# Optimization experiments

Measured on AMD Instinct MI355X. Metric: run time of the kernel, lower is better.

The kernel has to match this reference:

```python
import jax, jax.numpy as jnp
import numpy as np

B_, S_, P_, D_ = 2, 512, 64, 1024
L_ = 4            # n_layer
DI_ = 2 * D_      # d_inner (expand=2)
DS_ = 16          # d_state
DC_ = 4           # d_conv
DR_ = D_ // 16    # dt_rank
PCD_ = 768        # prepend_cond_dim


def setup_inputs() -> dict:
    key = jax.random.key(0)
    ks = jax.random.split(key, 12)
    n = lambda k, s, sc=0.02: jax.random.normal(k, s, dtype=jnp.float32) * sc
    A_log = jnp.log(jnp.broadcast_to(jnp.arange(1, DS_ + 1, dtype=jnp.float32), (L_, DI_, DS_)))
    return {
        'x': jax.random.normal(ks[0], (B_, S_, D_), dtype=jnp.float32),
        'prepend_cond': jax.random.normal(ks[1], (B_, P_, PCD_), dtype=jnp.float32),
        'pre_w1': n(ks[2], (PCD_, D_)),
        'pre_w2': n(ks[3], (D_, D_)),
        'norm_w': jnp.ones((L_, D_), jnp.float32),
        'in_proj_w': n(ks[4], (L_, 2 * DI_, D_)),
        'conv_w': n(ks[5], (L_, DI_, DC_), 0.1),
        'conv_b': jnp.zeros((L_, DI_), jnp.float32),
        'x_proj_w': n(ks[6], (L_, DR_ + 2 * DS_, DI_)),
        'dt_proj_w': n(ks[7], (L_, DI_, DR_), 0.1),
        'dt_proj_b': jax.random.uniform(ks[8], (L_, DI_), jnp.float32, -4.0, -2.0),
        'A_log': A_log,
        'D_param': jnp.ones((L_, DI_), jnp.float32),
        'out_proj_w': n(ks[9], (L_, D_, DI_)),
        'final_norm_w': jnp.ones((D_,), jnp.float32),
    }


def rmsnorm(x, w, eps=1e-5):
    return x * jax.lax.rsqrt(jnp.mean(x * x, axis=-1, keepdims=True) + eps) * w


def mamba_block(x, ip_w, cw, cb, xp_w, dtp_w, dtp_b, A_log, Dp, op_w):
    B, S, _ = x.shape
    xz = jnp.einsum('bsd,ed->bse', x, ip_w)            # [B,S,2*DI]
    xi, z = jnp.split(xz, 2, axis=-1)
    # depthwise causal conv1d along time
    xt = xi.transpose(0, 2, 1)                          # [B,DI,S]
    conv = jax.lax.conv_general_dilated(
        xt, cw[:, None, :], (1,), [(DC_ - 1, 0)], feature_group_count=DI_) + cb[:, None]
    xi = jax.nn.silu(conv.transpose(0, 2, 1))           # [B,S,DI]
    xdbl = jnp.einsum('bse,fe->bsf', xi, xp_w)          # [B,S,DR+2*DS]
    dt, Bm, Cm = jnp.split(xdbl, [DR_, DR_ + DS_], axis=-1)
    dt = jax.nn.softplus(jnp.einsum('bsr,er->bse', dt, dtp_w) + dtp_b)  # [B,S,DI]
    A = -jnp.exp(A_log)                                 # [DI,DS]
    dA = jnp.exp(dt[..., None] * A)                     # [B,S,DI,DS]
    dBu = dt[..., None] * Bm[:, :, None, :] * xi[..., None]

    def step(h, t):
        da, dbu, c = t
        h = da * h + dbu                                # [B,DI,DS]
        return h, jnp.einsum('bes,bs->be', h, c)

    h0 = jnp.zeros((B, DI_, DS_), x.dtype)
    _, ys = jax.lax.scan(step, h0, (dA.transpose(1, 0, 2, 3), dBu.transpose(1, 0, 2, 3), Cm.transpose(1, 0, 2)))
    y = ys.transpose(1, 0, 2) + xi * Dp
    y = y * jax.nn.silu(z)
    return jnp.einsum('bse,de->bsd', y, op_w)


def reference(x, prepend_cond, pre_w1, pre_w2, norm_w, in_proj_w, conv_w, conv_b,
              x_proj_w, dt_proj_w, dt_proj_b, A_log, D_param, out_proj_w, final_norm_w):
    p = jax.nn.silu(prepend_cond @ pre_w1) @ pre_w2     # to_prepend_embed
    h = jnp.concatenate([p, x], axis=1)                 # [B, P+S, D]
    for l in range(L_):
        h = h + mamba_block(rmsnorm(h, norm_w[l]), in_proj_w[l], conv_w[l], conv_b[l],
                            x_proj_w[l], dt_proj_w[l], dt_proj_b[l], A_log[l],
                            D_param[l], out_proj_w[l])
    h = rmsnorm(h, final_norm_w)
    return h[:, P_:, :]
```

## Files before the change

kernel.cpp:

```cpp
#include <hip/hip_runtime.h>
#include <math.h>

#define B_ 2
#define S_ 512
#define P_ 64
#define T_ 576
#define D_ 1024
#define L_ 4
#define DI_ 2048
#define DS_ 16
#define DC_ 4
#define DR_ 64
#define PCD_ 768
#define M_ (B_*T_)
#define CCH 18
#define NC (T_/CCH)
#define XKS 16

typedef __attribute__((ext_vector_type(8))) short bf16x8;
typedef __attribute__((ext_vector_type(4))) float f32x4;

__device__ __forceinline__ float silu_f(float v) { return v / (1.f + __expf(-v)); }
__device__ __forceinline__ float softplus_f(float v) {
    return fmaxf(v, 0.f) + log1pf(__expf(-fabsf(v)));
}
__device__ __forceinline__ unsigned short bf16_rne(float x) {
    unsigned int b = __float_as_uint(x);
    b += 0x7fffu + ((b >> 16) & 1u);
    return (unsigned short)(b >> 16);
}
__device__ __forceinline__ float bf16_to_f(unsigned short u) {
    return __uint_as_float((unsigned int)u << 16);
}

typedef const void __attribute__((address_space(1)))* gas_t;
typedef void __attribute__((address_space(3)))* las_t;
__device__ __forceinline__ void async16(const void* g, void* l) {
    __builtin_amdgcn_global_load_lds((gas_t)g, (las_t)l, 16, 0, 0);
}

template<int EPI>
__global__ __launch_bounds__(256) void gemm_mfma_kernel(
    const unsigned short* __restrict__ A, const unsigned short* __restrict__ W,
    float* __restrict__ C, float* __restrict__ C2,
    int M, int N, int K, int Kchunk)
{
    __shared__ unsigned short As[128 * 32];
    __shared__ unsigned short Bs[128 * 32];
    const int tid = threadIdx.x;
    const int wave = tid >> 6;
    const int lane = tid & 63;
    const int m0 = blockIdx.y * 128, n0 = blockIdx.x * 128;
    const int kbase = blockIdx.z * Kchunk;
    const int wm = (wave >> 1) * 64, wn = (wave & 1) * 64;

    const int srow = (wave << 5) + (lane >> 2);
    const int selem = (lane & 3) * 8;
    const unsigned short* gA = A + (size_t)(m0 + srow) * K + kbase + selem;
    const unsigned short* gB = W + (size_t)(n0 + srow) * K + kbase + selem;
    unsigned short* lA = As + (wave << 5) * 32;
    unsigned short* lB = Bs + (wave << 5) * 32;

    f32x4 acc[4][4];
    #pragma unroll
    for (int i = 0; i < 4; ++i)
        #pragma unroll
        for (int j = 0; j < 4; ++j)
            acc[i][j] = (f32x4){0.f, 0.f, 0.f, 0.f};

    const int fr = lane & 15;
    const int fq = lane >> 4;
    const int aoff = (wm + fr) * 32 + fq * 8;
    const int boff = (wn + fr) * 32 + fq * 8;

    for (int k0 = 0; k0 < Kchunk; k0 += 32) {
        async16(gA, lA);
        async16(gA + (size_t)16 * K, lA + 16 * 32);
        async16(gB, lB);
        async16(gB + (size_t)16 * K, lB + 16 * 32);
        gA += 32; gB += 32;
        __syncthreads();
        bf16x8 af[4], bf[4];
        #pragma unroll
        for (int i = 0; i < 4; ++i) af[i] = *(const bf16x8*)&As[aoff + i * 512];
        #pragma unroll
        for (int j = 0; j < 4; ++j) bf[j] = *(const bf16x8*)&Bs[boff + j * 512];
        #pragma unroll
        for (int i = 0; i < 4; ++i)
            #pragma unroll
            for (int j = 0; j < 4; ++j)
                acc[i][j] = __builtin_amdgcn_mfma_f32_16x16x32_bf16(
                    af[i], bf[j], acc[i][j], 0, 0, 0);
        __syncthreads();
    }

    #pragma unroll
    for (int i = 0; i < 4; ++i) {
        const int m = m0 + wm + i * 16 + fq * 4;
        #pragma unroll
        for (int j = 0; j < 4; ++j) {
            const int n = n0 + wn + j * 16 + fr;
            if (EPI == 6) {
                float* p = C + ((size_t)blockIdx.z * M + m) * N + n;
                #pragma unroll
                for (int r = 0; r < 4; ++r)
                    p[(size_t)r * N] = acc[i][j][r];
            } else if (EPI == 7) {
                if (n < DI_) {
                    float* p = C + (size_t)m * N + n;
                    #pragma unroll
                    for (int r = 0; r < 4; ++r)
                        p[(size_t)r * N] = acc[i][j][r];
                } else {
                    float* p = C2 + (size_t)m * DI_ + (n - DI_);
                    #pragma unroll
                    for (int r = 0; r < 4; ++r)
                        p[(size_t)r * DI_] = silu_f(acc[i][j][r]);
                }
            }
        }
    }
}

__global__ __launch_bounds__(256) void dtproj_kernel(
    const unsigned short* __restrict__ dtr,
    const unsigned short* __restrict__ Wb,
    const float* __restrict__ bias,
    float* __restrict__ dtb)
{
    __shared__ float As[16][DR_];
    const int tid = threadIdx.x;
    const int e = blockIdx.x * 256 + tid;
    const int m0 = blockIdx.y * 16;
    {
        const ushort4 a4 = ((const ushort4*)(dtr + (size_t)m0 * DR_))[tid];
        float* dst = &As[0][0] + tid * 4;
        dst[0] = bf16_to_f(a4.x);
        dst[1] = bf16_to_f(a4.y);
        dst[2] = bf16_to_f(a4.z);
        dst[3] = bf16_to_f(a4.w);
    }
    float w[DR_];
    {
        const ushort4* wp = (const ushort4*)(Wb + (size_t)e * DR_);
        #pragma unroll
        for (int q = 0; q < 16; ++q) {
            const ushort4 v = wp[q];
            w[q * 4 + 0] = bf16_to_f(v.x);
            w[q * 4 + 1] = bf16_to_f(v.y);
            w[q * 4 + 2] = bf16_to_f(v.z);
            w[q * 4 + 3] = bf16_to_f(v.w);
        }
    }
    __syncthreads();
    const float bb = bias[e];
    #pragma unroll
    for (int m = 0; m < 16; ++m) {
        float acc = 0.f;
        #pragma unroll
        for (int r = 0; r < DR_; ++r) acc = fmaf(As[m][r], w[r], acc);
        dtb[(size_t)(m0 + m) * DI_ + e] = softplus_f(acc + bb);
    }
}

__global__ __launch_bounds__(256) void xproj_mfma_kernel(
    const unsigned short* __restrict__ A,
    const unsigned short* __restrict__ W,
    float* __restrict__ P)
{
    __shared__ unsigned short As[128 * 32];
    __shared__ unsigned short Bs[96 * 32];
    const int tid = threadIdx.x;
    const int wave = tid >> 6;
    const int lane = tid & 63;
    const int m0 = blockIdx.y * 128;
    const int kbase = blockIdx.x * (DI_ / XKS);
    const int wm = (wave >> 1) * 64, wn = (wave & 1) * 48;

    const int srow = (wave << 5) + (lane >> 2);
    const int selem = (lane & 3) * 8;
    const unsigned short* gA = A + (size_t)(m0 + srow) * DI_ + kbase + selem;
    const unsigned short* gB = W + (size_t)srow * DI_ + kbase + selem;
    unsigned short* lA = As + (wave << 5) * 32;
    unsigned short* lB = Bs + (wave << 5) * 32;

    f32x4 acc[4][3];
    #pragma unroll
    for (int i = 0; i < 4; ++i)
        #pragma unroll
        for (int j = 0; j < 3; ++j)
            acc[i][j] = (f32x4){0.f, 0.f, 0.f, 0.f};

    const int fr = lane & 15;
    const int fq = lane >> 4;
    const int aoff = (wm + fr) * 32 + fq * 8;
    const int boff = (wn + fr) * 32 + fq * 8;

    #pragma unroll
    for (int kk = 0; kk < 4; ++kk) {
        async16(gA, lA);
        async16(gA + (size_t)16 * DI_, lA + 16 * 32);
        if (wave < 3) {
            async16(gB, lB);
            async16(gB + (size_t)16 * DI_, lB + 16 * 32);
        }
        gA += 32; gB += 32;
        __syncthreads();
        bf16x8 af[4], bf[3];
        #pragma unroll
        for (int i = 0; i < 4; ++i) af[i] = *(const bf16x8*)&As[aoff + i * 512];
        #pragma unroll
        for (int j = 0; j < 3; ++j) bf[j] = *(const bf16x8*)&Bs[boff + j * 512];
        #pragma unroll
        for (int i = 0; i < 4; ++i)
            #pragma unroll
            for (int j = 0; j < 3; ++j)
                acc[i][j] = __builtin_amdgcn_mfma_f32_16x16x32_bf16(
                    af[i], bf[j], acc[i][j], 0, 0, 0);
        __syncthreads();
    }

    float* Pb = P + ((size_t)blockIdx.x * M_ + m0) * 96;
    #pragma unroll
    for (int i = 0; i < 4; ++i) {
        const int m = wm + i * 16 + fq * 4;
        #pragma unroll
        for (int j = 0; j < 3; ++j) {
            const int n = wn + j * 16 + fr;
            #pragma unroll
            for (int r = 0; r < 4; ++r)
                Pb[(size_t)(m + r) * 96 + n] = acc[i][j][r];
        }
    }
}

__global__ __launch_bounds__(256) void xproj_reduce_kernel(
    const float* __restrict__ P, float* __restrict__ Bc, float* __restrict__ Cc,
    unsigned short* __restrict__ dtr_bf)
{
    const int i = blockIdx.x * 256 + threadIdx.x;
    if (i >= M_ * 96) return;
    float s = 0.f;
    #pragma unroll
    for (int ks = 0; ks < XKS; ++ks) s += P[(size_t)ks * (M_ * 96) + i];
    const int m = i / 96;
    const int n = i - m * 96;
    if (n < DR_)            dtr_bf[(size_t)m * DR_ + n] = bf16_rne(s);
    else if (n < DR_ + DS_) Bc[(size_t)m * DS_ + (n - DR_)] = s;
    else                    Cc[(size_t)m * DS_ + (n - DR_ - DS_)] = s;
}

__global__ __launch_bounds__(256) void cvt_bf16_kernel(
    const float* __restrict__ in, unsigned short* __restrict__ out, int n4)
{
    const int i = blockIdx.x * 256 + threadIdx.x;
    if (i >= n4) return;
    const float4 v = ((const float4*)in)[i];
    ushort4 o;
    o.x = bf16_rne(v.x); o.y = bf16_rne(v.y);
    o.z = bf16_rne(v.z); o.w = bf16_rne(v.w);
    ((ushort4*)out)[i] = o;
}

__global__ __launch_bounds__(256) void cvt4_kernel(
    const float* __restrict__ s0, unsigned short* __restrict__ d0, int n0,
    const float* __restrict__ s1, unsigned short* __restrict__ d1, int n1,
    const float* __restrict__ s2, unsigned short* __restrict__ d2, int n2,
    const float* __restrict__ s3, unsigned short* __restrict__ d3, int n3)
{
    const int i = blockIdx.x * 256 + threadIdx.x;
    const float* s; unsigned short* d; int off;
    if (i < n0)                { s = s0; d = d0; off = i; }
    else if (i < n0 + n1)      { s = s1; d = d1; off = i - n0; }
    else if (i < n0 + n1 + n2) { s = s2; d = d2; off = i - n0 - n1; }
    else if (i < n0 + n1 + n2 + n3) { s = s3; d = d3; off = i - n0 - n1 - n2; }
    else return;
    const float4 v = ((const float4*)s)[off];
    ushort4 o;
    o.x = bf16_rne(v.x); o.y = bf16_rne(v.y);
    o.z = bf16_rne(v.z); o.w = bf16_rne(v.w);
    ((ushort4*)d)[off] = o;
}

__global__ __launch_bounds__(256) void cvt_transpose_kernel(
    const float* __restrict__ in, unsigned short* __restrict__ out, int K, int N)
{
    __shared__ float t[64][65];
    const int k0 = blockIdx.x * 64;
    const int n0 = blockIdx.y * 64;
    const int tx = threadIdx.x & 63;
    const int ty = threadIdx.x >> 6;
    #pragma unroll
    for (int j = 0; j < 16; ++j) {
        const int kk = ty * 16 + j;
        t[kk][tx] = in[(size_t)(k0 + kk) * N + n0 + tx];
    }
    __syncthreads();
    #pragma unroll
    for (int j = 0; j < 16; ++j) {
        const int nn = ty * 16 + j;
        out[(size_t)(n0 + nn) * K + k0 + tx] = bf16_rne(t[tx][nn]);
    }
}

__global__ __launch_bounds__(256) void reduce_silu_bf16_kernel(
    const float* __restrict__ P, unsigned short* __restrict__ o, int MN, int ns)
{
    const int i = blockIdx.x * 256 + threadIdx.x;
    if (i >= MN) return;
    float s = 0.f;
    for (int k = 0; k < ns; ++k) s += P[(size_t)k * MN + i];
    o[i] = bf16_rne(silu_f(s));
}
__global__ __launch_bounds__(256) void reduce_fp32_kernel(
    const float* __restrict__ P, float* __restrict__ o, int MN, int ns)
{
    const int i = blockIdx.x * 256 + threadIdx.x;
    if (i >= MN) return;
    float s = 0.f;
    for (int k = 0; k < ns; ++k) s += P[(size_t)k * MN + i];
    o[i] = s;
}

__global__ __launch_bounds__(256) void outproj_rmsnorm_kernel(
    const float* __restrict__ P, float* __restrict__ h,
    const float* __restrict__ w, unsigned short* __restrict__ outb, int donorm)
{
    const int r = blockIdx.x;
    const int i = r * 256 + threadIdx.x;
    const float4 a4 = ((const float4*)P)[i];
    const float4 b4 = ((const float4*)P)[i + M_ * D_ / 4];
    float4 v = ((float4*)h)[i];
    v.x += a4.x + b4.x; v.y += a4.y + b4.y;
    v.z += a4.z + b4.z; v.w += a4.w + b4.w;
    ((float4*)h)[i] = v;
    if (!donorm) return;
    float ss = v.x * v.x + v.y * v.y + v.z * v.z + v.w * v.w;
    ss += __shfl_xor(ss, 32, 64);
    ss += __shfl_xor(ss, 16, 64);
    ss += __shfl_xor(ss, 8, 64);
    ss += __shfl_xor(ss, 4, 64);
    ss += __shfl_xor(ss, 2, 64);
    ss += __shfl_xor(ss, 1, 64);
    __shared__ float red[4];
    if ((threadIdx.x & 63) == 0) red[threadIdx.x >> 6] = ss;
    __syncthreads();
    const float tot = red[0] + red[1] + red[2] + red[3];
    const float scale = rsqrtf(tot * (1.f / D_) + 1e-5f);
    const float4 wv = ((const float4*)w)[threadIdx.x];
    ushort4 o;
    o.x = bf16_rne(v.x * scale * wv.x);
    o.y = bf16_rne(v.y * scale * wv.y);
    o.z = bf16_rne(v.z * scale * wv.z);
    o.w = bf16_rne(v.w * scale * wv.w);
    ((ushort4*)(outb + (size_t)r * D_))[threadIdx.x] = o;
}

__global__ __launch_bounds__(256) void assemble_h_kernel(
    const float* __restrict__ p, const float* __restrict__ x, float* __restrict__ h)
{
    const int idx = blockIdx.x * 256 + threadIdx.x;
    const int r = idx >> 8;
    const int c = idx & 255;
    const int b = r / T_;
    const int t = r - b * T_;
    float4 v;
    if (t < P_) v = ((const float4*)p)[(size_t)(b * P_ + t) * 256 + c];
    else        v = ((const float4*)x)[(size_t)(b * S_ + (t - P_)) * 256 + c];
    ((float4*)h)[idx] = v;
}

__global__ __launch_bounds__(256) void rmsnorm_bf16_kernel(
    const float* __restrict__ x, const float* __restrict__ w,
    unsigned short* __restrict__ outb)
{
    const int r = blockIdx.x;
    const float4 v = ((const float4*)(x + (size_t)r * D_))[threadIdx.x];
    float ss = v.x * v.x + v.y * v.y + v.z * v.z + v.w * v.w;
    ss += __shfl_xor(ss, 32, 64);
    ss += __shfl_xor(ss, 16, 64);
    ss += __shfl_xor(ss, 8, 64);
    ss += __shfl_xor(ss, 4, 64);
    ss += __shfl_xor(ss, 2, 64);
    ss += __shfl_xor(ss, 1, 64);
    __shared__ float red[4];
    if ((threadIdx.x & 63) == 0) red[threadIdx.x >> 6] = ss;
    __syncthreads();
    const float tot = red[0] + red[1] + red[2] + red[3];
    const float scale = rsqrtf(tot * (1.f / D_) + 1e-5f);
    const float4 wv = ((const float4*)w)[threadIdx.x];
    ushort4 o;
    o.x = bf16_rne(v.x * scale * wv.x);
    o.y = bf16_rne(v.y * scale * wv.y);
    o.z = bf16_rne(v.z * scale * wv.z);
    o.w = bf16_rne(v.w * scale * wv.w);
    ((ushort4*)(outb + (size_t)r * D_))[threadIdx.x] = o;
}

__global__ __launch_bounds__(256) void final_rmsnorm_kernel(
    const float* __restrict__ h, const float* __restrict__ w, float* __restrict__ out)
{
    const int r = blockIdx.x;
    const int b = r / S_;
    const int s = r - b * S_;
    const int hr = b * T_ + P_ + s;
    const float4 v = ((const float4*)(h + (size_t)hr * D_))[threadIdx.x];
    float ss = v.x * v.x + v.y * v.y + v.z * v.z + v.w * v.w;
    ss += __shfl_xor(ss, 32, 64);
    ss += __shfl_xor(ss, 16, 64);
    ss += __shfl_xor(ss, 8, 64);
    ss += __shfl_xor(ss, 4, 64);
    ss += __shfl_xor(ss, 2, 64);
    ss += __shfl_xor(ss, 1, 64);
    __shared__ float red[4];
    if ((threadIdx.x & 63) == 0) red[threadIdx.x >> 6] = ss;
    __syncthreads();
    const float tot = red[0] + red[1] + red[2] + red[3];
    const float scale = rsqrtf(tot * (1.f / D_) + 1e-5f);
    const float4 wv = ((const float4*)w)[threadIdx.x];
    float4 o;
    o.x = v.x * scale * wv.x; o.y = v.y * scale * wv.y;
    o.z = v.z * scale * wv.z; o.w = v.w * scale * wv.w;
    ((float4*)(out + (size_t)r * D_))[threadIdx.x] = o;
}

__global__ __launch_bounds__(256) void conv_silu_kernel(
    const float* __restrict__ xz, const float* __restrict__ cw,
    const float* __restrict__ cb, unsigned short* __restrict__ xib,
    float* __restrict__ xim)
{
    __shared__ float xs[67][64];
    const int tid = threadIdx.x;
    const int tx = tid & 63;
    const int ty = tid >> 6;
    const int r0 = blockIdx.x * 64;
    const int e0 = blockIdx.y * 64;
    const int bt0 = (r0 / T_) * T_;

    for (int j = ty; j < 67; j += 4) {
        const int r = r0 + j - 3;
        xs[j][tx] = (r >= bt0) ? xz[(size_t)r * (2 * DI_) + e0 + tx] : 0.f;
    }
    __syncthreads();
    const float4 w = *(const float4*)(cw + (size_t)(e0 + tx) * 4);
    const float bias = cb[e0 + tx];
    #pragma unroll
    for (int j = 0; j < 16; ++j) {
        const int rl = ty * 16 + j;
        float v = bias;
        v = fmaf(w.x, xs[rl + 0][tx], v);
        v = fmaf(w.y, xs[rl + 1][tx], v);
        v = fmaf(w.z, xs[rl + 2][tx], v);
        v = fmaf(w.w, xs[rl + 3][tx], v);
        const float o = silu_f(v);
        const size_t go = (size_t)(r0 + rl) * DI_ + e0 + tx;
        xib[go] = bf16_rne(o);
        xim[go] = o;
    }
}

__global__ __launch_bounds__(256) void scan_chunk1_kernel(
    const float* __restrict__ dtm,
    const float* __restrict__ Bc,
    const float* __restrict__ xim,
    const float* __restrict__ A_log,
    float* __restrict__ Ap, float* __restrict__ Hp)
{
    __shared__ float4 Bs[CCH][4];
    const int tid = threadIdx.x;
    const int e = ((blockIdx.x & 7) << 8) + tid;
    const int cb = blockIdx.x >> 3;
    const int b = cb & (B_ - 1);
    const int c = cb >> 1;
    const int r0 = b * T_ + c * CCH;
    for (int i = tid; i < CCH * DS_; i += 256)
        ((float*)Bs)[i] = Bc[(size_t)r0 * DS_ + i];
    float A2[DS_], h[DS_], a[DS_];
    const float* Ae = A_log + (size_t)e * DS_;
    #pragma unroll
    for (int s = 0; s < DS_; ++s) {
        A2[s] = -__expf(Ae[s]) * 1.44269504f;
        h[s] = 0.f; a[s] = 1.f;
    }
    __syncthreads();
    const float* dp = dtm + (size_t)r0 * DI_ + e;
    const float* up = xim + (size_t)r0 * DI_ + e;
    #pragma unroll
    for (int t = 0; t < CCH; ++t) {
        const float dtv = dp[(size_t)t * DI_];
        const float dtu = dtv * up[(size_t)t * DI_];
        #pragma unroll
        for (int q = 0; q < 4; ++q) {
            const float4 bq = Bs[t][q];
            const float* bb = &bq.x;
            #pragma unroll
            for (int j = 0; j < 4; ++j) {
                const int s = q * 4 + j;
                const float da = __builtin_amdgcn_exp2f(dtv * A2[s]);
                a[s] *= da;
                h[s] = fmaf(da, h[s], bb[j] * dtu);
            }
        }
    }
    const size_t o = (size_t)cb * DS_ * DI_ + e;
    #pragma unroll
    for (int s = 0; s < DS_; ++s) {
        Ap[o + (size_t)s * DI_] = a[s];
        Hp[o + (size_t)s * DI_] = h[s];
    }
}

__global__ __launch_bounds__(256) void scan_chunk2_kernel(
    float* __restrict__ Ap, float* __restrict__ Hp)
{
    const int g = blockIdx.x * 256 + threadIdx.x;
    float h = 0.f;
    #pragma unroll
    for (int c = 0; c < NC; ++c) {
        const size_t o = (size_t)c * (B_ * DI_ * DS_) + g;
        const float ap = Ap[o];
        const float hp = Hp[o];
        Hp[o] = h;
        h = fmaf(ap, h, hp);
    }
}

__global__ __launch_bounds__(256) void scan_chunk3_kernel(
    const float* __restrict__ dtm,
    const float* __restrict__ Bc,
    const float* __restrict__ Cc,
    const float* __restrict__ xim,
    const float* __restrict__ szm,
    const float* __restrict__ A_log, const float* __restrict__ Dp,
    const float* __restrict__ Hin, unsigned short* __restrict__ y)
{
    __shared__ float4 Bs[CCH][4], Cs[CCH][4];
    const int tid = threadIdx.x;
    const int e = ((blockIdx.x & 7) << 8) + tid;
    const int cb = blockIdx.x >> 3;
    const int b = cb & (B_ - 1);
    const int c = cb >> 1;
    const int r0 = b * T_ + c * CCH;
    for (int i = tid; i < CCH * DS_; i += 256) {
        ((float*)Bs)[i] = Bc[(size_t)r0 * DS_ + i];
        ((float*)Cs)[i] = Cc[(size_t)r0 * DS_ + i];
    }
    float A2[DS_], h[DS_];
    const float* Ae = A_log + (size_t)e * DS_;
    const float dpe = Dp[e];
    const size_t ho = (size_t)cb * DS_ * DI_ + e;
    #pragma unroll
    for (int s = 0; s < DS_; ++s) {
        A2[s] = -__expf(Ae[s]) * 1.44269504f;
        h[s] = Hin[ho + (size_t)s * DI_];
    }
    __syncthreads();
    const float* dp = dtm + (size_t)r0 * DI_ + e;
    const float* up = xim + (size_t)r0 * DI_ + e;
    const float* sp = szm + (size_t)r0 * DI_ + e;
    unsigned short* yp = y + (size_t)r0 * DI_ + e;
    #pragma unroll
    for (int t = 0; t < CCH; ++t) {
        const float dtv = dp[(size_t)t * DI_];
        const float u   = up[(size_t)t * DI_];
        const float dtu = dtv * u;
        float y0 = 0.f, y1 = 0.f, y2 = 0.f, y3 = 0.f;
        #pragma unroll
        for (int q = 0; q < 4; ++q) {
            const float4 bq = Bs[t][q];
            const float4 cq = Cs[t][q];
            const float* bb = &bq.x;
            const float* cc = &cq.x;
            #pragma unroll
            for (int j = 0; j < 4; ++j) {
                const int s = q * 4 + j;
                const float da = __builtin_amdgcn_exp2f(dtv * A2[s]);
                h[s] = fmaf(da, h[s], bb[j] * dtu);
                if (j == 0)      y0 = fmaf(h[s], cc[j], y0);
                else if (j == 1) y1 = fmaf(h[s], cc[j], y1);
                else if (j == 2) y2 = fmaf(h[s], cc[j], y2);
                else             y3 = fmaf(h[s], cc[j], y3);
            }
        }
        const float ysum = (y0 + y1) + (y2 + y3);
        const float yv = fmaf(u, dpe, ysum) * sp[(size_t)t * DI_];
        yp[(size_t)t * DI_] = bf16_rne(yv);
    }
}

extern "C" void kernel_launch(void* const* d_in, const int* in_sizes, int n_in,
                              void* d_out, int out_size, void* d_ws, size_t ws_size,
                              hipStream_t stream)
{
    const float* x       = (const float*)d_in[0];
    const float* pc      = (const float*)d_in[1];
    const float* pre_w1  = (const float*)d_in[2];
    const float* pre_w2  = (const float*)d_in[3];
    const float* norm_w  = (const float*)d_in[4];
    const float* ip_w    = (const float*)d_in[5];
    const float* conv_w  = (const float*)d_in[6];
    const float* conv_b  = (const float*)d_in[7];
    const float* xp_w    = (const float*)d_in[8];
    const float* dtp_w   = (const float*)d_in[9];
    const float* dtp_b   = (const float*)d_in[10];
    const float* A_log   = (const float*)d_in[11];
    const float* D_param = (const float*)d_in[12];
    const float* op_w    = (const float*)d_in[13];
    const float* fnw     = (const float*)d_in[14];
    float* out = (float*)d_out;

    float* ws = (float*)d_ws;
    float* h    = ws;  ws += (size_t)M_ * D_;
    float* xz   = ws;  ws += (size_t)M_ * 2 * DI_;
    float* xim  = ws;  ws += (size_t)M_ * DI_;
    float* szm  = ws;  ws += (size_t)M_ * DI_;
    float* dtb  = ws;  ws += (size_t)M_ * DI_;
    float* Pbuf = ws;  ws += (size_t)XKS * M_ * 96;
    float* Bc   = ws;  ws += (size_t)DS_ * M_;
    float* Cc   = ws;  ws += (size_t)DS_ * M_;
    unsigned short* xn_bf  = (unsigned short*)ws;  ws += (size_t)M_ * D_ / 2;
    unsigned short* yb_bf  = (unsigned short*)ws;  ws += (size_t)M_ * DI_ / 2;
    unsigned short* xi_bf  = (unsigned short*)ws;  ws += (size_t)M_ * DI_ / 2;
    unsigned short* dtr_bf = (unsigned short*)ws;  ws += (size_t)M_ * DR_ / 2;
    unsigned short* wbuf   = (unsigned short*)ws;  ws += (size_t)2 * DI_ * D_ / 2;
    unsigned short* xpw_bf = (unsigned short*)ws;  ws += (size_t)96 * DI_ / 2;
    unsigned short* dtpw_bf= (unsigned short*)ws;  ws += (size_t)DI_ * DR_ / 2;
    unsigned short* opw_bf = (unsigned short*)ws;  ws += (size_t)D_ * DI_ / 2;

    float* Ap = xz;
    float* Hp = xz + (size_t)NC * B_ * DI_ * DS_;

    unsigned short* pc_bf   = xi_bf;
    unsigned short* w1t_bf  = wbuf;
    unsigned short* w2t_bf  = wbuf + (size_t)D_ * PCD_;
    unsigned short* tmp1_bf = xn_bf;
    float*          tmp2    = szm;
    float*          Pop     = xz;

    const dim3 blk(256);

    cvt_bf16_kernel<<<dim3(B_ * P_ * PCD_ / 4 / 256), blk, 0, stream>>>(
        pc, pc_bf, B_ * P_ * PCD_ / 4);
    cvt_transpose_kernel<<<dim3(PCD_ / 64, D_ / 64), blk, 0, stream>>>(
        pre_w1, w1t_bf, PCD_, D_);
    cvt_transpose_kernel<<<dim3(D_ / 64, D_ / 64), blk, 0, stream>>>(
        pre_w2, w2t_bf, D_, D_);
    gemm_mfma_kernel<6><<<dim3(D_ / 128, 1, 6), blk, 0, stream>>>(
        pc_bf, w1t_bf, Pbuf, nullptr, B_ * P_, D_, PCD_, PCD_ / 6);
    reduce_silu_bf16_kernel<<<dim3(B_ * P_ * D_ / 256), blk, 0, stream>>>(
        Pbuf, tmp1_bf, B_ * P_ * D_, 6);
    gemm_mfma_kernel<6><<<dim3(D_ / 128, 1, 8), blk, 0, stream>>>(
        tmp1_bf, w2t_bf, Pbuf, nullptr, B_ * P_, D_, D_, D_ / 8);
    reduce_fp32_kernel<<<dim3(B_ * P_ * D_ / 256), blk, 0, stream>>>(
        Pbuf, tmp2, B_ * P_ * D_, 8);
    assemble_h_kernel<<<dim3(M_ * D_ / 4 / 256), blk, 0, stream>>>(tmp2, x, h);

    const int n_ip  = 2 * DI_ * D_ / 4;
    const int n_xp  = 96 * DI_ / 4;
    const int n_dtp = DI_ * DR_ / 4;
    const int n_op  = D_ * DI_ / 4;

    rmsnorm_bf16_kernel<<<dim3(M_), blk, 0, stream>>>(h, norm_w, xn_bf);

    for (int l = 0; l < L_; ++l) {
        cvt4_kernel<<<dim3((n_ip + n_xp + n_dtp + n_op + 255) / 256), blk, 0, stream>>>(
            ip_w + (size_t)l * 2 * DI_ * D_, wbuf, n_ip,
            xp_w + (size_t)l * 96 * DI_, xpw_bf, n_xp,
            dtp_w + (size_t)l * DI_ * DR_, dtpw_bf, n_dtp,
            op_w + (size_t)l * D_ * DI_, opw_bf, n_op);
        gemm_mfma_kernel<7><<<dim3(2 * DI_ / 128, M_ / 128, 1), blk, 0, stream>>>(
            xn_bf, wbuf, xz, szm, M_, 2 * DI_, D_, D_);
        conv_silu_kernel<<<dim3(M_ / 64, DI_ / 64), blk, 0, stream>>>(
            xz, conv_w + (size_t)l * DI_ * DC_, conv_b + (size_t)l * DI_,
            xi_bf, xim);
        xproj_mfma_kernel<<<dim3(XKS, M_ / 128), blk, 0, stream>>>(
            xi_bf, xpw_bf, Pbuf);
        xproj_reduce_kernel<<<dim3((M_ * 96 + 255) / 256), blk, 0, stream>>>(
            Pbuf, Bc, Cc, dtr_bf);
        dtproj_kernel<<<dim3(DI_ / 256, M_ / 16), blk, 0, stream>>>(
            dtr_bf, dtpw_bf, dtp_b + (size_t)l * DI_, dtb);
        scan_chunk1_kernel<<<dim3(NC * B_ * DI_ / 256), blk, 0, stream>>>(
            dtb, Bc, xim, A_log + (size_t)l * DI_ * DS_, Ap, Hp);
        scan_chunk2_kernel<<<dim3(B_ * DI_ * DS_ / 256), blk, 0, stream>>>(Ap, Hp);
        scan_chunk3_kernel<<<dim3(NC * B_ * DI_ / 256), blk, 0, stream>>>(
            dtb, Bc, Cc, xim, szm, A_log + (size_t)l * DI_ * DS_,
            D_param + (size_t)l * DI_, Hp, yb_bf);
        gemm_mfma_kernel<6><<<dim3(D_ / 128, M_ / 128, 2), blk, 0, stream>>>(
            yb_bf, opw_bf, Pop, nullptr, M_, D_, DI_, DI_ / 2);
        outproj_rmsnorm_kernel<<<dim3(M_), blk, 0, stream>>>(
            Pop, h, norm_w + (size_t)((l + 1) & 3) * D_, xn_bf, l < L_ - 1);
    }

    final_rmsnorm_kernel<<<dim3(B_ * S_), blk, 0, stream>>>(h, fnw, out);
}
```

Measured before the change: 745.2 us.

## Store in_proj outputs and conv activations as bf16, deepen split-K for GEMMs

The in_proj GEMM epilogue now writes the x-half and silu(z) as bf16 instead of fp32. The conv and scan kernels read bf16 activations, and the fp32 xim and szm buffers are dropped. This cuts global memory traffic for several large M×DI intermediates, at the cost of bf16 rounding on inputs the scan used to read in fp32. Split-K factors are also raised for the out_proj GEMM (now 4) and the prepend GEMMs to expose more parallelism, which adds more partial-sum reduction traffic. Workspace aliasing is adjusted so tmp2 uses Pbuf and the second prepend GEMM's partials use dtb.

New measurement: 740.4 us. Within noise of the previous version (-0.6%).

```diff
diff --git a/kernel.cpp b/kernel.cpp
--- a/kernel.cpp
+++ b/kernel.cpp
@@ -16,6 +16,7 @@
 #define CCH 18
 #define NC (T_/CCH)
 #define XKS 16
+#define OPK 4
 
 typedef __attribute__((ext_vector_type(8))) short bf16x8;
 typedef __attribute__((ext_vector_type(4))) float f32x4;
@@ -107,15 +108,15 @@
                     p[(size_t)r * N] = acc[i][j][r];
             } else if (EPI == 7) {
                 if (n < DI_) {
-                    float* p = C + (size_t)m * N + n;
+                    unsigned short* p = (unsigned short*)C + (size_t)m * DI_ + n;
                     #pragma unroll
                     for (int r = 0; r < 4; ++r)
-                        p[(size_t)r * N] = acc[i][j][r];
+                        p[(size_t)r * DI_] = bf16_rne(acc[i][j][r]);
                 } else {
-                    float* p = C2 + (size_t)m * DI_ + (n - DI_);
+                    unsigned short* p = (unsigned short*)C2 + (size_t)m * DI_ + (n - DI_);
                     #pragma unroll
                     for (int r = 0; r < 4; ++r)
-                        p[(size_t)r * DI_] = silu_f(acc[i][j][r]);
+                        p[(size_t)r * DI_] = bf16_rne(silu_f(acc[i][j][r]));
                 }
             }
         }
@@ -328,11 +329,12 @@
 {
     const int r = blockIdx.x;
     const int i = r * 256 + threadIdx.x;
-    const float4 a4 = ((const float4*)P)[i];
-    const float4 b4 = ((const float4*)P)[i + M_ * D_ / 4];
     float4 v = ((float4*)h)[i];
-    v.x += a4.x + b4.x; v.y += a4.y + b4.y;
-    v.z += a4.z + b4.z; v.w += a4.w + b4.w;
+    #pragma unroll
+    for (int k = 0; k < OPK; ++k) {
+        const float4 a4 = ((const float4*)P)[i + k * (M_ * D_ / 4)];
+        v.x += a4.x; v.y += a4.y; v.z += a4.z; v.w += a4.w;
+    }
     ((float4*)h)[i] = v;
     if (!donorm) return;
     float ss = v.x * v.x + v.y * v.y + v.z * v.z + v.w * v.w;
@@ -425,9 +427,8 @@
 }
 
 __global__ __launch_bounds__(256) void conv_silu_kernel(
-    const float* __restrict__ xz, const float* __restrict__ cw,
-    const float* __restrict__ cb, unsigned short* __restrict__ xib,
-    float* __restrict__ xim)
+    const unsigned short* __restrict__ xb, const float* __restrict__ cw,
+    const float* __restrict__ cb, unsigned short* __restrict__ xib)
 {
     __shared__ float xs[67][64];
     const int tid = threadIdx.x;
@@ -439,7 +440,7 @@
 
     for (int j = ty; j < 67; j += 4) {
         const int r = r0 + j - 3;
-        xs[j][tx] = (r >= bt0) ? xz[(size_t)r * (2 * DI_) + e0 + tx] : 0.f;
+        xs[j][tx] = (r >= bt0) ? bf16_to_f(xb[(size_t)r * DI_ + e0 + tx]) : 0.f;
     }
     __syncthreads();
     const float4 w = *(const float4*)(cw + (size_t)(e0 + tx) * 4);
@@ -452,17 +453,14 @@
         v = fmaf(w.y, xs[rl + 1][tx], v);
         v = fmaf(w.z, xs[rl + 2][tx], v);
         v = fmaf(w.w, xs[rl + 3][tx], v);
-        const float o = silu_f(v);
-        const size_t go = (size_t)(r0 + rl) * DI_ + e0 + tx;
-        xib[go] = bf16_rne(o);
-        xim[go] = o;
+        xib[(size_t)(r0 + rl) * DI_ + e0 + tx] = bf16_rne(silu_f(v));
     }
 }
 
 __global__ __launch_bounds__(256) void scan_chunk1_kernel(
     const float* __restrict__ dtm,
     const float* __restrict__ Bc,
-    const float* __restrict__ xim,
+    const unsigned short* __restrict__ xib,
     const float* __restrict__ A_log,
     float* __restrict__ Ap, float* __restrict__ Hp)
 {
@@ -484,11 +482,11 @@
     }
     __syncthreads();
     const float* dp = dtm + (size_t)r0 * DI_ + e;
-    const float* up = xim + (size_t)r0 * DI_ + e;
+    const unsigned short* up = xib + (size_t)r0 * DI_ + e;
     #pragma unroll
     for (int t = 0; t < CCH; ++t) {
         const float dtv = dp[(size_t)t * DI_];
-        const float dtu = dtv * up[(size_t)t * DI_];
+        const float dtu = dtv * bf16_to_f(up[(size_t)t * DI_]);
         #pragma unroll
         for (int q = 0; q < 4; ++q) {
             const float4 bq = Bs[t][q];
@@ -529,8 +527,8 @@
     const float* __restrict__ dtm,
     const float* __restrict__ Bc,
     const float* __restrict__ Cc,
-    const float* __restrict__ xim,
-    const float* __restrict__ szm,
+    const unsigned short* __restrict__ xib,
+    const unsigned short* __restrict__ szb,
     const float* __restrict__ A_log, const float* __restrict__ Dp,
     const float* __restrict__ Hin, unsigned short* __restrict__ y)
 {
@@ -556,13 +554,13 @@
     }
     __syncthreads();
     const float* dp = dtm + (size_t)r0 * DI_ + e;
-    const float* up = xim + (size_t)r0 * DI_ + e;
-    const float* sp = szm + (size_t)r0 * DI_ + e;
+    const unsigned short* up = xib + (size_t)r0 * DI_ + e;
+    const unsigned short* sp = szb + (size_t)r0 * DI_ + e;
     unsigned short* yp = y + (size_t)r0 * DI_ + e;
     #pragma unroll
     for (int t = 0; t < CCH; ++t) {
         const float dtv = dp[(size_t)t * DI_];
-        const float u   = up[(size_t)t * DI_];
+        const float u   = bf16_to_f(up[(size_t)t * DI_]);
         const float dtu = dtv * u;
         float y0 = 0.f, y1 = 0.f, y2 = 0.f, y3 = 0.f;
         #pragma unroll
@@ -583,7 +581,7 @@
             }
         }
         const float ysum = (y0 + y1) + (y2 + y3);
-        const float yv = fmaf(u, dpe, ysum) * sp[(size_t)t * DI_];
+        const float yv = fmaf(u, dpe, ysum) * bf16_to_f(sp[(size_t)t * DI_]);
         yp[(size_t)t * DI_] = bf16_rne(yv);
     }
 }
@@ -612,8 +610,6 @@
     float* ws = (float*)d_ws;
     float* h    = ws;  ws += (size_t)M_ * D_;
     float* xz   = ws;  ws += (size_t)M_ * 2 * DI_;
-    float* xim  = ws;  ws += (size_t)M_ * DI_;
-    float* szm  = ws;  ws += (size_t)M_ * DI_;
     float* dtb  = ws;  ws += (size_t)M_ * DI_;
     float* Pbuf = ws;  ws += (size_t)XKS * M_ * 96;
     float* Bc   = ws;  ws += (size_t)DS_ * M_;
@@ -621,6 +617,8 @@
     unsigned short* xn_bf  = (unsigned short*)ws;  ws += (size_t)M_ * D_ / 2;
     unsigned short* yb_bf  = (unsigned short*)ws;  ws += (size_t)M_ * DI_ / 2;
     unsigned short* xi_bf  = (unsigned short*)ws;  ws += (size_t)M_ * DI_ / 2;
+    unsigned short* xb_bf  = (unsigned short*)ws;  ws += (size_t)M_ * DI_ / 2;
+    unsigned short* szb_bf = (unsigned short*)ws;  ws += (size_t)M_ * DI_ / 2;
     unsigned short* dtr_bf = (unsigned short*)ws;  ws += (size_t)M_ * DR_ / 2;
     unsigned short* wbuf   = (unsigned short*)ws;  ws += (size_t)2 * DI_ * D_ / 2;
     unsigned short* xpw_bf = (unsigned short*)ws;  ws += (size_t)96 * DI_ / 2;
@@ -634,7 +632,8 @@
     unsigned short* w1t_bf  = wbuf;
     unsigned short* w2t_bf  = wbuf + (size_t)D_ * PCD_;
     unsigned short* tmp1_bf = xn_bf;
-    float*          tmp2    = szm;
+    float*          tmp2    = Pbuf;
+    float*          P2buf   = dtb;
     float*          Pop     = xz;
 
     const dim3 blk(256);
@@ -645,14 +644,14 @@
         pre_w1, w1t_bf, PCD_, D_);
     cvt_transpose_kernel<<<dim3(D_ / 64, D_ / 64), blk, 0, stream>>>(
         pre_w2, w2t_bf, D_, D_);
-    gemm_mfma_kernel<6><<<dim3(D_ / 128, 1, 6), blk, 0, stream>>>(
-        pc_bf, w1t_bf, Pbuf, nullptr, B_ * P_, D_, PCD_, PCD_ / 6);
+    gemm_mfma_kernel<6><<<dim3(D_ / 128, 1, 12), blk, 0, stream>>>(
+        pc_bf, w1t_bf, Pbuf, nullptr, B_ * P_, D_, PCD_, PCD_ / 12);
     reduce_silu_bf16_kernel<<<dim3(B_ * P_ * D_ / 256), blk, 0, stream>>>(
-        Pbuf, tmp1_bf, B_ * P_ * D_, 6);
-    gemm_mfma_kernel<6><<<dim3(D_ / 128, 1, 8), blk, 0, stream>>>(
-        tmp1_bf, w2t_bf, Pbuf, nullptr, B_ * P_, D_, D_, D_ / 8);
+        Pbuf, tmp1_bf, B_ * P_ * D_, 12);
+    gemm_mfma_kernel<6><<<dim3(D_ / 128, 1, 16), blk, 0, stream>>>(
+        tmp1_bf, w2t_bf, P2buf, nullptr, B_ * P_, D_, D_, D_ / 16);
     reduce_fp32_kernel<<<dim3(B_ * P_ * D_ / 256), blk, 0, stream>>>(
-        Pbuf, tmp2, B_ * P_ * D_, 8);
+        P2buf, tmp2, B_ * P_ * D_, 16);
     assemble_h_kernel<<<dim3(M_ * D_ / 4 / 256), blk, 0, stream>>>(tmp2, x, h);
 
     const int n_ip  = 2 * DI_ * D_ / 4;
@@ -669,10 +668,10 @@
             dtp_w + (size_t)l * DI_ * DR_, dtpw_bf, n_dtp,
             op_w + (size_t)l * D_ * DI_, opw_bf, n_op);
         gemm_mfma_kernel<7><<<dim3(2 * DI_ / 128, M_ / 128, 1), blk, 0, stream>>>(
-            xn_bf, wbuf, xz, szm, M_, 2 * DI_, D_, D_);
+            xn_bf, wbuf, (float*)xb_bf, (float*)szb_bf, M_, 2 * DI_, D_, D_);
         conv_silu_kernel<<<dim3(M_ / 64, DI_ / 64), blk, 0, stream>>>(
-            xz, conv_w + (size_t)l * DI_ * DC_, conv_b + (size_t)l * DI_,
-            xi_bf, xim);
+            xb_bf, conv_w + (size_t)l * DI_ * DC_, conv_b + (size_t)l * DI_,
+            xi_bf);
         xproj_mfma_kernel<<<dim3(XKS, M_ / 128), blk, 0, stream>>>(
             xi_bf, xpw_bf, Pbuf);
         xproj_reduce_kernel<<<dim3((M_ * 96 + 255) / 256), blk, 0, stream>>>(
@@ -680,13 +679,13 @@
         dtproj_kernel<<<dim3(DI_ / 256, M_ / 16), blk, 0, stream>>>(
             dtr_bf, dtpw_bf, dtp_b + (size_t)l * DI_, dtb);
         scan_chunk1_kernel<<<dim3(NC * B_ * DI_ / 256), blk, 0, stream>>>(
-            dtb, Bc, xim, A_log + (size_t)l * DI_ * DS_, Ap, Hp);
+            dtb, Bc, xi_bf, A_log + (size_t)l * DI_ * DS_, Ap, Hp);
         scan_chunk2_kernel<<<dim3(B_ * DI_ * DS_ / 256), blk, 0, stream>>>(Ap, Hp);
         scan_chunk3_kernel<<<dim3(NC * B_ * DI_ / 256), blk, 0, stream>>>(
-            dtb, Bc, Cc, xim, szm, A_log + (size_t)l * DI_ * DS_,
+            dtb, Bc, Cc, xi_bf, szb_bf, A_log + (size_t)l * DI_ * DS_,
             D_param + (size_t)l * DI_, Hp, yb_bf);
-        gemm_mfma_kernel<6><<<dim3(D_ / 128, M_ / 128, 2), blk, 0, stream>>>(
-            yb_bf, opw_bf, Pop, nullptr, M_, D_, DI_, DI_ / 2);
+        gemm_mfma_kernel<6><<<dim3(D_ / 128, M_ / 128, OPK), blk, 0, stream>>>(
+            yb_bf, opw_bf, Pop, nullptr, M_, D_, DI_, DI_ / OPK);
         outproj_rmsnorm_kernel<<<dim3(M_), blk, 0, stream>>>(
             Pop, h, norm_w + (size_t)((l + 1) & 3) * D_, xn_bf, l < L_ - 1);
     }
```
